# Optimization experiments

Hardware: AMD Instinct MI355X
Metric: run time of the kernel (lower is better)

Reference implementation:

```python
import jax, jax.numpy as jnp
import numpy as np

IN_CH = 4          # qubits
KSZ = 3            # kernel size
NUM_KERNELS = 2
LAYERS = 1
STRIDE = 1
DILATION = 1
NPOS = KSZ * KSZ
TOTAL_W = NPOS * LAYERS * IN_CH * 3  # 108


def setup_inputs() -> dict:
    key = jax.random.key(0)
    k1, k2 = jax.random.split(key)
    x = jax.random.normal(k1, (16, IN_CH, 64, 64), dtype=jnp.float32)
    weights = jax.random.uniform(k2, (NUM_KERNELS, TOTAL_W), minval=-np.pi, maxval=np.pi, dtype=jnp.float32)
    return {"x": x, "weights": weights}


def _apply_1q(state, U, q):
    # state: (N, 2,...,2) with IN_CH qubit axes; U: (2,2) shared or (N,2,2) batched
    s = jnp.moveaxis(state, q + 1, -1)
    if U.ndim == 2:
        s = jnp.einsum('ab,...b->...a', U, s)
    else:
        s = jnp.einsum('nab,n...b->n...a', U, s)
    return jnp.moveaxis(s, -1, q + 1)


def _ry_mat(theta):
    c = jnp.cos(theta / 2)
    s = jnp.sin(theta / 2)
    return jnp.stack([jnp.stack([c, -s], -1), jnp.stack([s, c], -1)], -2).astype(jnp.complex64)


def _rx_mat(theta):
    c = jnp.cos(theta / 2).astype(jnp.complex64)
    s = (-1j) * jnp.sin(theta / 2).astype(jnp.complex64)
    return jnp.stack([jnp.stack([c, s], -1), jnp.stack([s, c], -1)], -2)


def _rz_mat(theta):
    e = jnp.exp((-0.5j) * theta.astype(jnp.complex64))
    z = jnp.zeros_like(e)
    return jnp.stack([jnp.stack([e, z], -1), jnp.stack([z, jnp.conj(e)], -1)], -2)


def _cx(state, cq, tq):
    s = jnp.moveaxis(state, (cq + 1, tq + 1), (-2, -1))
    s = s.at[..., 1, :].set(s[..., 1, ::-1])  # flip target where control=1
    return jnp.moveaxis(s, (-2, -1), (cq + 1, tq + 1))


def _circuit(w_flat, patches):
    # patches: (N, IN_CH, NPOS) data angles; w_flat: (TOTAL_W,)
    n = IN_CH
    N = patches.shape[0]
    dim = 2 ** n
    # H on every qubit from |0...0> == uniform superposition with + amplitudes
    state = jnp.full((N,) + (2,) * n, 1.0 / np.sqrt(dim), dtype=jnp.complex64)
    w = w_flat.reshape(NPOS, LAYERS, n, 3)
    for pos in range(NPOS):
        for ch in range(n):
            state = _apply_1q(state, _ry_mat(patches[:, ch, pos]), ch)
        for l in range(LAYERS):
            for q in range(n):
                state = _apply_1q(state, _rx_mat(w[pos, l, q, 0]), q)
                state = _apply_1q(state, _ry_mat(w[pos, l, q, 1]), q)
                state = _apply_1q(state, _rz_mat(w[pos, l, q, 2]), q)
            for q in range(n - 1):
                state = _cx(state, q, q + 1)
            if n > 1:
                state = _cx(state, n - 1, 0)
    p = jnp.abs(state) ** 2  # (N, 2,...,2)
    sign = jnp.array([1.0, -1.0], dtype=jnp.float32)
    exps = []
    for q in range(n):
        sh = [1] * (n + 1)
        sh[q + 1] = 2
        exps.append(jnp.sum(p * sign.reshape(sh), axis=tuple(range(1, n + 1))))
    return jnp.stack(exps, -1)  # (N, n) <Z_q> expectations


def _extract_patches(x):
    B, C, H, W = x.shape
    out_h = (H - (KSZ - 1) * DILATION - 1) // STRIDE + 1
    out_w = (W - (KSZ - 1) * DILATION - 1) // STRIDE + 1
    hh = (jnp.arange(out_h) * STRIDE)[:, None] + jnp.arange(KSZ)[None, :] * DILATION  # (out_h, K)
    ww = (jnp.arange(out_w) * STRIDE)[:, None] + jnp.arange(KSZ)[None, :] * DILATION  # (out_w, K)
    p = x[:, :, hh][:, :, :, :, ww]                  # (B, C, out_h, K, out_w, K)
    p = p.transpose(0, 2, 4, 1, 3, 5)                # (B, out_h, out_w, C, K, K)
    return p.reshape(B, out_h * out_w, C, KSZ * KSZ), out_h, out_w


def reference(x, weights):
    B, C, H, W = x.shape
    patches, out_h, out_w = _extract_patches(x)
    flat = patches.reshape(B * out_h * out_w, C, KSZ * KSZ)
    outs = []
    for kidx in range(NUM_KERNELS):
        e = _circuit(weights[kidx], flat)                       # (B*P, C)
        e = e.reshape(B, out_h, out_w, C).transpose(0, 3, 1, 2)  # (B, C, out_h, out_w)
        outs.append(e)
    return jnp.concatenate(outs, axis=1)  # (B, NUM_KERNELS*C, out_h, out_w)
```

## Files before the change

### kernel.cpp

```cpp
#include <hip/hip_runtime.h>
#include <math.h>

#define IN_CH 4
#define KSZ 3
#define NUM_KERNELS 2
#define NPOS 9
#define HH 64
#define WW 64
#define BB 16
#define OH 62
#define OW 62
#define NPATCH (BB*OH*OW)
#define NU (NPOS*IN_CH)
#define UFLOATS (NU*8)

__global__ void qk_precompute(const float* __restrict__ w, float* __restrict__ U) {
    int t = blockIdx.x * blockDim.x + threadIdx.x;
    if (t >= NUM_KERNELS * NU) return;
    int k   = t / NU;
    int rem = t % NU;
    const float* wp = w + k * (NU * 3) + rem * 3;
    float hx = 0.5f * wp[0], hy = 0.5f * wp[1], hz = 0.5f * wp[2];
    float cx = cosf(hx), sx = sinf(hx);
    float cy = cosf(hy), sy = sinf(hy);
    float cz = cosf(hz), sz = sinf(hz);
    float m00r =  cy * cx, m00i =  sy * sx;
    float m01r = -sy * cx, m01i = -cy * sx;
    float m10r =  sy * cx, m10i = -cy * sx;
    float m11r =  cy * cx, m11i = -sy * sx;
    float* o = U + t * 8;
    o[0] = cz * m00r + sz * m00i;  o[1] = cz * m00i - sz * m00r;
    o[2] = cz * m01r + sz * m01i;  o[3] = cz * m01i - sz * m01r;
    o[4] = cz * m10r - sz * m10i;  o[5] = cz * m10i + sz * m10r;
    o[6] = cz * m11r - sz * m11i;  o[7] = cz * m11i + sz * m11r;
}

__global__ __launch_bounds__(256) void qk_main(const float* __restrict__ x,
                                               const float* __restrict__ Uglob,
                                               float* __restrict__ out) {
    __shared__ float sU[UFLOATS];
    const int kidx = blockIdx.y;
    const int tid  = threadIdx.x;
    for (int t = tid; t < UFLOATS; t += 256) sU[t] = Uglob[kidx * UFLOATS + t];
    __syncthreads();

    int p = blockIdx.x * 256 + tid;
    if (p >= NPATCH) return;
    int b   = p / (OH * OW);
    int rem = p - b * (OH * OW);
    int oh  = rem / OW;
    int ow  = rem - oh * OW;
    const float* xb = x + b * (IN_CH * HH * WW);

    float sr[16], si[16];
    #pragma unroll
    for (int i = 0; i < 16; ++i) { sr[i] = 0.25f; si[i] = 0.0f; }

    #pragma unroll
    for (int kh = 0; kh < KSZ; ++kh) {
        #pragma unroll
        for (int kw = 0; kw < KSZ; ++kw) {
            const int pos = kh * KSZ + kw;
            #pragma unroll
            for (int ch = 0; ch < IN_CH; ++ch) {
                float th = xb[ch * (HH * WW) + (oh + kh) * WW + (ow + kw)];
                float s, c;
                __sincosf(0.5f * th, &s, &c);
                const int mask = 8 >> ch;
                #pragma unroll
                for (int i = 0; i < 16; ++i) {
                    if (i & mask) continue;
                    const int j = i | mask;
                    float ar = sr[i], ai = si[i], br = sr[j], bi = si[j];
                    sr[i] = c * ar - s * br;  si[i] = c * ai - s * bi;
                    sr[j] = s * ar + c * br;  si[j] = s * ai + c * bi;
                }
            }
            #pragma unroll
            for (int q = 0; q < IN_CH; ++q) {
                const float* u = &sU[(pos * IN_CH + q) * 8];
                const float u00r = u[0], u00i = u[1], u01r = u[2], u01i = u[3];
                const float u10r = u[4], u10i = u[5], u11r = u[6], u11i = u[7];
                const int mask = 8 >> q;
                #pragma unroll
                for (int i = 0; i < 16; ++i) {
                    if (i & mask) continue;
                    const int j = i | mask;
                    float ar = sr[i], ai = si[i], br = sr[j], bi = si[j];
                    sr[i] = u00r * ar - u00i * ai + u01r * br - u01i * bi;
                    si[i] = u00r * ai + u00i * ar + u01r * bi + u01i * br;
                    sr[j] = u10r * ar - u10i * ai + u11r * br - u11i * bi;
                    si[j] = u10r * ai + u10i * ar + u11r * bi + u11i * br;
                }
            }
            #pragma unroll
            for (int e = 0; e < 4; ++e) {
                const int cmask = 8 >> e;
                const int tmask = 8 >> ((e + 1) & 3);
                #pragma unroll
                for (int i = 0; i < 16; ++i) {
                    if ((i & cmask) && !(i & tmask)) {
                        const int j = i | tmask;
                        float tr = sr[i]; sr[i] = sr[j]; sr[j] = tr;
                        float ti = si[i]; si[i] = si[j]; si[j] = ti;
                    }
                }
            }
        }
    }

    float p2[16];
    #pragma unroll
    for (int i = 0; i < 16; ++i) p2[i] = sr[i] * sr[i] + si[i] * si[i];

    float* ob = out + ((size_t)(b * (NUM_KERNELS * IN_CH) + kidx * IN_CH) * OH + oh) * OW + ow;
    #pragma unroll
    for (int q = 0; q < IN_CH; ++q) {
        const int mask = 8 >> q;
        float e = 0.0f;
        #pragma unroll
        for (int i = 0; i < 16; ++i) e += (i & mask) ? -p2[i] : p2[i];
        ob[q * (OH * OW)] = e;
    }
}

extern "C" void kernel_launch(void* const* d_in, const int* in_sizes, int n_in,
                              void* d_out, int out_size, void* d_ws, size_t ws_size,
                              hipStream_t stream) {
    const float* x = (const float*)d_in[0];
    const float* w = (const float*)d_in[1];
    float* out = (float*)d_out;
    float* U   = (float*)d_ws;

    hipLaunchKernelGGL(qk_precompute, dim3(1), dim3(128), 0, stream, w, U);
    dim3 grid((NPATCH + 255) / 256, NUM_KERNELS);
    hipLaunchKernelGGL(qk_main, grid, dim3(256), 0, stream, x, U, out);
}
```

Measured before the change: 77.70 us.

## Fold data RY rotation into weight unitary and prefetch patch inputs

Each per-qubit data RY gate is multiplied into the precomputed weight unitary, giving one fused 2x2 complex matrix per qubit per position. This replaces two passes over the 16-amplitude state with one, roughly halving the arithmetic of that section. All 36 patch values are loaded into registers up front so load latency can overlap, and the block size drops from 256 to 64. The trade-offs are higher register pressure and a higher ratio of the shared-memory unitary copy per thread.

```diff
diff --git a/kernel.cpp b/kernel.cpp
--- a/kernel.cpp
+++ b/kernel.cpp
@@ -13,6 +13,7 @@
 #define NPATCH (BB*OH*OW)
 #define NU (NPOS*IN_CH)
 #define UFLOATS (NU*8)
+#define BLK 64
 
 __global__ void qk_precompute(const float* __restrict__ w, float* __restrict__ U) {
     int t = blockIdx.x * blockDim.x + threadIdx.x;
@@ -35,75 +36,71 @@
     o[6] = cz * m11r - sz * m11i;  o[7] = cz * m11i + sz * m11r;
 }
 
-__global__ __launch_bounds__(256) void qk_main(const float* __restrict__ x,
+__global__ __launch_bounds__(BLK) void qk_main(const float* __restrict__ x,
                                                const float* __restrict__ Uglob,
                                                float* __restrict__ out) {
     __shared__ float sU[UFLOATS];
     const int kidx = blockIdx.y;
     const int tid  = threadIdx.x;
-    for (int t = tid; t < UFLOATS; t += 256) sU[t] = Uglob[kidx * UFLOATS + t];
+    for (int t = tid; t < UFLOATS; t += BLK) sU[t] = Uglob[kidx * UFLOATS + t];
     __syncthreads();
 
-    int p = blockIdx.x * 256 + tid;
+    int p = blockIdx.x * BLK + tid;
     if (p >= NPATCH) return;
     int b   = p / (OH * OW);
     int rem = p - b * (OH * OW);
     int oh  = rem / OW;
     int ow  = rem - oh * OW;
-    const float* xb = x + b * (IN_CH * HH * WW);
+    const float* xb = x + b * (IN_CH * HH * WW) + oh * WW + ow;
+
+    float xv[NPOS * IN_CH];
+    #pragma unroll
+    for (int ch = 0; ch < IN_CH; ++ch)
+        #pragma unroll
+        for (int kh = 0; kh < KSZ; ++kh)
+            #pragma unroll
+            for (int kw = 0; kw < KSZ; ++kw)
+                xv[(kh * KSZ + kw) * IN_CH + ch] = xb[ch * (HH * WW) + kh * WW + kw];
 
     float sr[16], si[16];
     #pragma unroll
     for (int i = 0; i < 16; ++i) { sr[i] = 0.25f; si[i] = 0.0f; }
 
     #pragma unroll
-    for (int kh = 0; kh < KSZ; ++kh) {
+    for (int pos = 0; pos < NPOS; ++pos) {
         #pragma unroll
-        for (int kw = 0; kw < KSZ; ++kw) {
-            const int pos = kh * KSZ + kw;
+        for (int q = 0; q < IN_CH; ++q) {
+            float s, c;
+            __sincosf(0.5f * xv[pos * IN_CH + q], &s, &c);
+            const float* u = &sU[(pos * IN_CH + q) * 8];
+            const float u00r = u[0], u00i = u[1], u01r = u[2], u01i = u[3];
+            const float u10r = u[4], u10i = u[5], u11r = u[6], u11i = u[7];
+            const float f00r = c * u00r + s * u01r, f00i = c * u00i + s * u01i;
+            const float f10r = c * u10r + s * u11r, f10i = c * u10i + s * u11i;
+            const float f01r = c * u01r - s * u00r, f01i = c * u01i - s * u00i;
+            const float f11r = c * u11r - s * u10r, f11i = c * u11i - s * u10i;
+            const int mask = 8 >> q;
             #pragma unroll
-            for (int ch = 0; ch < IN_CH; ++ch) {
-                float th = xb[ch * (HH * WW) + (oh + kh) * WW + (ow + kw)];
-                float s, c;
-                __sincosf(0.5f * th, &s, &c);
-                const int mask = 8 >> ch;
-                #pragma unroll
-                for (int i = 0; i < 16; ++i) {
-                    if (i & mask) continue;
-                    const int j = i | mask;
-                    float ar = sr[i], ai = si[i], br = sr[j], bi = si[j];
-                    sr[i] = c * ar - s * br;  si[i] = c * ai - s * bi;
-                    sr[j] = s * ar + c * br;  si[j] = s * ai + c * bi;
-                }
+            for (int i = 0; i < 16; ++i) {
+                if (i & mask) continue;
+                const int j = i | mask;
+                float ar = sr[i], ai = si[i], br = sr[j], bi = si[j];
+                sr[i] = f00r * ar - f00i * ai + f01r * br - f01i * bi;
+                si[i] = f00r * ai + f00i * ar + f01r * bi + f01i * br;
+                sr[j] = f10r * ar - f10i * ai + f11r * br - f11i * bi;
+                si[j] = f10r * ai + f10i * ar + f11r * bi + f11i * br;
             }
+        }
+        #pragma unroll
+        for (int e = 0; e < 4; ++e) {
+            const int cmask = 8 >> e;
+            const int tmask = 8 >> ((e + 1) & 3);
             #pragma unroll
-            for (int q = 0; q < IN_CH; ++q) {
-                const float* u = &sU[(pos * IN_CH + q) * 8];
-                const float u00r = u[0], u00i = u[1], u01r = u[2], u01i = u[3];
-                const float u10r = u[4], u10i = u[5], u11r = u[6], u11i = u[7];
-                const int mask = 8 >> q;
-                #pragma unroll
-                for (int i = 0; i < 16; ++i) {
-                    if (i & mask) continue;
-                    const int j = i | mask;
-                    float ar = sr[i], ai = si[i], br = sr[j], bi = si[j];
-                    sr[i] = u00r * ar - u00i * ai + u01r * br - u01i * bi;
-                    si[i] = u00r * ai + u00i * ar + u01r * bi + u01i * br;
-                    sr[j] = u10r * ar - u10i * ai + u11r * br - u11i * bi;
-                    si[j] = u10r * ai + u10i * ar + u11r * bi + u11i * br;
-                }
-            }
-            #pragma unroll
-            for (int e = 0; e < 4; ++e) {
-                const int cmask = 8 >> e;
-                const int tmask = 8 >> ((e + 1) & 3);
-                #pragma unroll
-                for (int i = 0; i < 16; ++i) {
-                    if ((i & cmask) && !(i & tmask)) {
-                        const int j = i | tmask;
-                        float tr = sr[i]; sr[i] = sr[j]; sr[j] = tr;
-                        float ti = si[i]; si[i] = si[j]; si[j] = ti;
-                    }
+            for (int i = 0; i < 16; ++i) {
+                if ((i & cmask) && !(i & tmask)) {
+                    const int j = i | tmask;
+                    float tr = sr[i]; sr[i] = sr[j]; sr[j] = tr;
+                    float ti = si[i]; si[i] = si[j]; si[j] = ti;
                 }
             }
         }
@@ -133,6 +130,6 @@
     float* U   = (float*)d_ws;
 
     hipLaunchKernelGGL(qk_precompute, dim3(1), dim3(128), 0, stream, w, U);
-    dim3 grid((NPATCH + 255) / 256, NUM_KERNELS);
-    hipLaunchKernelGGL(qk_main, grid, dim3(256), 0, stream, x, U, out);
+    dim3 grid((NPATCH + BLK - 1) / BLK, NUM_KERNELS);
+    hipLaunchKernelGGL(qk_main, grid, dim3(BLK), 0, stream, x, U, out);
 }
```

Measured after the change: 74.79 us. 1.04x faster.

## Fuse data RY into weight unitary and evaluate both kernels per thread

Applied to the files above, without the earlier changes.

Folds each data-dependent RY rotation into the precomputed weight unitary (using SU(2) structure so only 4 floats per gate are stored), which halves the per-qubit gate applications. Each thread now simulates both kernels' circuits for the same patch, so the input loads and sincos are shared instead of being done twice across blockIdx.y. Block size drops to 64 and the bounds check is removed, relying on NPATCH being divisible by 64. Keeping two 16-amplitude complex states live doubles register pressure, which may lower occupancy.

```diff
diff --git a/kernel.cpp b/kernel.cpp
--- a/kernel.cpp
+++ b/kernel.cpp
@@ -12,7 +12,9 @@
 #define OW 62
 #define NPATCH (BB*OH*OW)
 #define NU (NPOS*IN_CH)
-#define UFLOATS (NU*8)
+#define CHST (HH*WW)
+#define BLK 64
+#define UF4 (NUM_KERNELS*NU*4)
 
 __global__ void qk_precompute(const float* __restrict__ w, float* __restrict__ U) {
     int t = blockIdx.x * blockDim.x + threadIdx.x;
@@ -26,35 +28,63 @@
     float cz = cosf(hz), sz = sinf(hz);
     float m00r =  cy * cx, m00i =  sy * sx;
     float m01r = -sy * cx, m01i = -cy * sx;
-    float m10r =  sy * cx, m10i = -cy * sx;
-    float m11r =  cy * cx, m11i = -sy * sx;
-    float* o = U + t * 8;
+    float* o = U + t * 4;
     o[0] = cz * m00r + sz * m00i;  o[1] = cz * m00i - sz * m00r;
     o[2] = cz * m01r + sz * m01i;  o[3] = cz * m01i - sz * m01r;
-    o[4] = cz * m10r - sz * m10i;  o[5] = cz * m10i + sz * m10r;
-    o[6] = cz * m11r - sz * m11i;  o[7] = cz * m11i + sz * m11r;
 }
 
-__global__ __launch_bounds__(256) void qk_main(const float* __restrict__ x,
+__device__ __forceinline__ void gate2(float sr[16], float si[16], const int mask,
+                                      const float far_, const float fai,
+                                      const float fbr, const float fbi) {
+    #pragma unroll
+    for (int i = 0; i < 16; ++i) {
+        if (i & mask) continue;
+        const int j = i | mask;
+        float ar = sr[i], ai = si[i], br = sr[j], bi = si[j];
+        sr[i] =  far_ * ar - fai * ai + fbr * br - fbi * bi;
+        si[i] =  far_ * ai + fai * ar + fbr * bi + fbi * br;
+        sr[j] = -fbr * ar - fbi * ai + far_ * br + fai * bi;
+        si[j] =  fbi * ar - fbr * ai - fai * br + far_ * bi;
+    }
+}
+
+__device__ __forceinline__ void cx_ring(float sr[16], float si[16]) {
+    #pragma unroll
+    for (int e = 0; e < 4; ++e) {
+        const int cmask = 8 >> e;
+        const int tmask = 8 >> ((e + 1) & 3);
+        #pragma unroll
+        for (int i = 0; i < 16; ++i) {
+            if ((i & cmask) && !(i & tmask)) {
+                const int j = i | tmask;
+                float tr = sr[i]; sr[i] = sr[j]; sr[j] = tr;
+                float ti = si[i]; si[i] = si[j]; si[j] = ti;
+            }
+        }
+    }
+}
+
+__global__ __launch_bounds__(BLK) void qk_main(const float* __restrict__ x,
                                                const float* __restrict__ Uglob,
                                                float* __restrict__ out) {
-    __shared__ float sU[UFLOATS];
-    const int kidx = blockIdx.y;
-    const int tid  = threadIdx.x;
-    for (int t = tid; t < UFLOATS; t += 256) sU[t] = Uglob[kidx * UFLOATS + t];
+    __shared__ float sU[UF4];
+    const int tid = threadIdx.x;
+    for (int t = tid; t < UF4; t += BLK) sU[t] = Uglob[t];
     __syncthreads();
 
-    int p = blockIdx.x * 256 + tid;
-    if (p >= NPATCH) return;
-    int b   = p / (OH * OW);
-    int rem = p - b * (OH * OW);
-    int oh  = rem / OW;
-    int ow  = rem - oh * OW;
-    const float* xb = x + b * (IN_CH * HH * WW);
+    const int p   = blockIdx.x * BLK + tid;
+    const int b   = p / (OH * OW);
+    const int rem = p - b * (OH * OW);
+    const int oh  = rem / OW;
+    const int ow  = rem - oh * OW;
+    const float* xp = x + b * (IN_CH * CHST) + oh * WW + ow;
 
-    float sr[16], si[16];
+    float s0r[16], s0i[16], s1r[16], s1i[16];
     #pragma unroll
-    for (int i = 0; i < 16; ++i) { sr[i] = 0.25f; si[i] = 0.0f; }
+    for (int i = 0; i < 16; ++i) {
+        s0r[i] = 0.25f; s0i[i] = 0.0f;
+        s1r[i] = 0.25f; s1i[i] = 0.0f;
+    }
 
     #pragma unroll
     for (int kh = 0; kh < KSZ; ++kh) {
@@ -62,65 +92,48 @@
         for (int kw = 0; kw < KSZ; ++kw) {
             const int pos = kh * KSZ + kw;
             #pragma unroll
-            for (int ch = 0; ch < IN_CH; ++ch) {
-                float th = xb[ch * (HH * WW) + (oh + kh) * WW + (ow + kw)];
+            for (int q = 0; q < IN_CH; ++q) {
+                const float th = xp[q * CHST + kh * WW + kw];
                 float s, c;
                 __sincosf(0.5f * th, &s, &c);
-                const int mask = 8 >> ch;
-                #pragma unroll
-                for (int i = 0; i < 16; ++i) {
-                    if (i & mask) continue;
-                    const int j = i | mask;
-                    float ar = sr[i], ai = si[i], br = sr[j], bi = si[j];
-                    sr[i] = c * ar - s * br;  si[i] = c * ai - s * bi;
-                    sr[j] = s * ar + c * br;  si[j] = s * ai + c * bi;
+                const int mask = 8 >> q;
+                {
+                    const float* u = &sU[(pos * IN_CH + q) * 4];
+                    const float far_ = c * u[0] + s * u[2], fai = c * u[1] + s * u[3];
+                    const float fbr  = c * u[2] - s * u[0], fbi = c * u[3] - s * u[1];
+                    gate2(s0r, s0i, mask, far_, fai, fbr, fbi);
+                }
+                {
+                    const float* u = &sU[(NU + pos * IN_CH + q) * 4];
+                    const float far_ = c * u[0] + s * u[2], fai = c * u[1] + s * u[3];
+                    const float fbr  = c * u[2] - s * u[0], fbi = c * u[3] - s * u[1];
+                    gate2(s1r, s1i, mask, far_, fai, fbr, fbi);
                 }
             }
-            #pragma unroll
-            for (int q = 0; q < IN_CH; ++q) {
-                const float* u = &sU[(pos * IN_CH + q) * 8];
-                const float u00r = u[0], u00i = u[1], u01r = u[2], u01i = u[3];
-                const float u10r = u[4], u10i = u[5], u11r = u[6], u11i = u[7];
-                const int mask = 8 >> q;
-                #pragma unroll
-                for (int i = 0; i < 16; ++i) {
-                    if (i & mask) continue;
-                    const int j = i | mask;
-                    float ar = sr[i], ai = si[i], br = sr[j], bi = si[j];
-                    sr[i] = u00r * ar - u00i * ai + u01r * br - u01i * bi;
-                    si[i] = u00r * ai + u00i * ar + u01r * bi + u01i * br;
-                    sr[j] = u10r * ar - u10i * ai + u11r * br - u11i * bi;
-                    si[j] = u10r * ai + u10i * ar + u11r * bi + u11i * br;
-                }
-            }
-            #pragma unroll
-            for (int e = 0; e < 4; ++e) {
-                const int cmask = 8 >> e;
-                const int tmask = 8 >> ((e + 1) & 3);
-                #pragma unroll
-                for (int i = 0; i < 16; ++i) {
-                    if ((i & cmask) && !(i & tmask)) {
-                        const int j = i | tmask;
-                        float tr = sr[i]; sr[i] = sr[j]; sr[j] = tr;
-                        float ti = si[i]; si[i] = si[j]; si[j] = ti;
-                    }
-                }
-            }
+            cx_ring(s0r, s0i);
+            cx_ring(s1r, s1i);
         }
     }
 
-    float p2[16];
+    float p20[16], p21[16];
     #pragma unroll
-    for (int i = 0; i < 16; ++i) p2[i] = sr[i] * sr[i] + si[i] * si[i];
+    for (int i = 0; i < 16; ++i) {
+        p20[i] = s0r[i] * s0r[i] + s0i[i] * s0i[i];
+        p21[i] = s1r[i] * s1r[i] + s1i[i] * s1i[i];
+    }
 
-    float* ob = out + ((size_t)(b * (NUM_KERNELS * IN_CH) + kidx * IN_CH) * OH + oh) * OW + ow;
+    float* ob = out + ((size_t)(b * (NUM_KERNELS * IN_CH)) * OH + oh) * OW + ow;
     #pragma unroll
     for (int q = 0; q < IN_CH; ++q) {
         const int mask = 8 >> q;
-        float e = 0.0f;
+        float e0 = 0.0f, e1 = 0.0f;
         #pragma unroll
-        for (int i = 0; i < 16; ++i) e += (i & mask) ? -p2[i] : p2[i];
-        ob[q * (OH * OW)] = e;
+        for (int i = 0; i < 16; ++i) {
+            e0 += (i & mask) ? -p20[i] : p20[i];
+            e1 += (i & mask) ? -p21[i] : p21[i];
+        }
+        ob[(size_t)q * (OH * OW)]            = e0;
+        ob[(size_t)(IN_CH + q) * (OH * OW)]  = e1;
     }
 }
 
@@ -133,6 +146,5 @@
     float* U   = (float*)d_ws;
 
     hipLaunchKernelGGL(qk_precompute, dim3(1), dim3(128), 0, stream, w, U);
-    dim3 grid((NPATCH + 255) / 256, NUM_KERNELS);
-    hipLaunchKernelGGL(qk_main, grid, dim3(256), 0, stream, x, U, out);
+    hipLaunchKernelGGL(qk_main, dim3(NPATCH / BLK), dim3(BLK), 0, stream, x, U, out);
 }
```

Result: no change. 78.80 us (+1.4%).
